# Performance work log

Measured on AMD Instinct MI355X. Metric: run time of the kernel, lower is better.

## Reference

```python
import jax, jax.numpy as jnp
import numpy as np

B, S, H, NH = 4, 1024, 2048, 16
D = H // NH  # head_dim = 128


def setup_inputs() -> dict:
    key = jax.random.key(0)
    ks = jax.random.split(key, 10)
    # RoPE tables: angle[t, j] = t * 10000^(-2j/D), cos/sin of the complex freqs_cis
    t = jnp.arange(S, dtype=jnp.float32)
    inv_freq = 1.0 / (10000.0 ** (jnp.arange(0, D, 2, dtype=jnp.float32) / D))
    ang = t[:, None] * inv_freq[None, :]  # [S, D//2]
    w = 0.02
    return {
        "hidden_states": jax.random.normal(ks[0], (B, S, H), jnp.float32),
        "freqs_cos": jnp.cos(ang),
        "freqs_sin": jnp.sin(ang),
        "attention_mask": jnp.ones((B, 1, 1, S), jnp.float32),
        "Wq": jax.random.normal(ks[1], (H, H), jnp.float32) * w,
        "bq": jnp.zeros((H,), jnp.float32),
        "Wk": jax.random.normal(ks[2], (H, H), jnp.float32) * w,
        "bk": jnp.zeros((H,), jnp.float32),
        "Wv": jax.random.normal(ks[3], (H, H), jnp.float32) * w,
        "bv": jnp.zeros((H,), jnp.float32),
        "Wo": jax.random.normal(ks[4], (H, H), jnp.float32) * w,
        "bo": jnp.zeros((H,), jnp.float32),
    }


def _rope(x, cos, sin):
    # x: [B, S, NH, D]; cos/sin: [S, D//2]. Complex multiply on (even, odd) pairs.
    x2 = x.reshape(x.shape[:-1] + (D // 2, 2))
    x0, x1 = x2[..., 0], x2[..., 1]
    c = cos[None, :, None, :]
    s = sin[None, :, None, :]
    o0 = x0 * c - x1 * s
    o1 = x0 * s + x1 * c
    return jnp.stack([o0, o1], axis=-1).reshape(x.shape)


def reference(hidden_states, freqs_cos, freqs_sin, attention_mask,
              Wq, bq, Wk, bk, Wv, bv, Wo, bo):
    b, s, _ = hidden_states.shape
    q = (hidden_states @ Wq.T + bq).reshape(b, s, NH, D)
    k = (hidden_states @ Wk.T + bk).reshape(b, s, NH, D)
    v = (hidden_states @ Wv.T + bv).reshape(b, s, NH, D)
    q = _rope(q, freqs_cos, freqs_sin)
    k = _rope(k, freqs_cos, freqs_sin)
    # scores: [b, h, q, k]; original scales by sqrt(embed_dim)=sqrt(hidden_size)
    scores = jnp.einsum('bqhd,bkhd->bhqk', q, k) / jnp.sqrt(jnp.float32(H))
    scores = jnp.where(attention_mask == 0, jnp.float32(-1e9), scores)
    probs = jax.nn.softmax(scores, axis=-1)  # dropout is identity in eval
    ctx = jnp.einsum('bhqk,bkhd->bqhd', probs, v).reshape(b, s, H)
    return ctx @ Wo.T + bo
```

## Files before the change

### kernel.cpp

```cpp
#include <hip/hip_runtime.h>
#include <stdint.h>

#define BATCH 4
#define SEQ   1024
#define NHEAD 16
#define DHEAD 128
#define HDIM  2048
#define GM    4096
#define GN    2048
#define GK    2048

typedef __attribute__((ext_vector_type(8)))  short    short8;
typedef __attribute__((ext_vector_type(4)))  float    f32x4;
typedef __attribute__((ext_vector_type(16))) float    f32x16;
typedef __attribute__((ext_vector_type(4)))  uint32_t u32x4;

__device__ __forceinline__ uint16_t f2bf(float f) {
  uint32_t u = __builtin_bit_cast(uint32_t, f);
  u += 0x7fffu + ((u >> 16) & 1u);
  return (uint16_t)(u >> 16);
}
__device__ __forceinline__ float bf2f(uint16_t h) {
  return __builtin_bit_cast(float, (uint32_t)h << 16);
}
__device__ __forceinline__ uint32_t cvtpk(float lo, float hi) {
  uint32_t r;
  asm("v_cvt_pk_bf16_f32 %0, %1, %2" : "=v"(r) : "v"(lo), "v"(hi));
  return r;
}

__device__ __forceinline__ uint32_t swz128(uint32_t a) { return a ^ (((a >> 7) & 7u) << 4); }
__device__ __forceinline__ uint32_t swz256(uint32_t a) { return a ^ (((a >> 8) & 7u) << 4); }

#define GAS __attribute__((address_space(1)))
#define LAS __attribute__((address_space(3)))
__device__ __forceinline__ void gload_lds16(const void* g, void* l) {
  __builtin_amdgcn_global_load_lds((GAS const void*)g, (LAS void*)l, 16, 0, 0);
}

__global__ void cvt_all_kernel(const float* __restrict__ hs,
                               const float* __restrict__ W0, const float* __restrict__ W1,
                               const float* __restrict__ W2, const float* __restrict__ W3,
                               uint16_t* __restrict__ Xbf, uint16_t* __restrict__ Wb) {
  const int bid = blockIdx.x;
  const float* src; uint16_t* dst;
  if (bid < 4096) {
    src = hs + (size_t)bid * 2048;
    dst = Xbf + (size_t)bid * 2048;
  } else {
    const int m = (bid - 4096) >> 11;
    const int blk = (bid - 4096) & 2047;
    const float* Ws = (m == 0) ? W0 : (m == 1) ? W1 : (m == 2) ? W2 : W3;
    src = Ws + (size_t)blk * 2048;
    dst = Wb + (size_t)m * HDIM * HDIM + (size_t)blk * 2048;
  }
  const float4* p = (const float4*)src + (size_t)threadIdx.x * 2;
  float4 a = p[0], b = p[1];
  uint32_t w0 = f2bf(a.x) | ((uint32_t)f2bf(a.y) << 16);
  uint32_t w1 = f2bf(a.z) | ((uint32_t)f2bf(a.w) << 16);
  uint32_t w2 = f2bf(b.x) | ((uint32_t)f2bf(b.y) << 16);
  uint32_t w3 = f2bf(b.z) | ((uint32_t)f2bf(b.w) << 16);
  int4 r; r.x = (int)w0; r.y = (int)w1; r.z = (int)w2; r.w = (int)w3;
  *(int4*)(dst + (size_t)threadIdx.x * 8) = r;
}

__global__ void rope_kernel(uint16_t* __restrict__ qb, uint16_t* __restrict__ kb,
                            const float* __restrict__ fcos, const float* __restrict__ fsin) {
  uint32_t i = blockIdx.x * 256 + threadIdx.x;
  uint16_t* p = (blockIdx.y == 0 ? qb : kb) + (size_t)i * 8;
  uint32_t e0 = i * 8;
  uint32_t row = e0 >> 11;
  uint32_t col = e0 & 2047;
  uint32_t s = row & (SEQ - 1);
  uint32_t pi = (col & (DHEAD - 1)) >> 1;
  float4 cv = *(const float4*)(fcos + (size_t)s * 64 + pi);
  float4 sv = *(const float4*)(fsin + (size_t)s * 64 + pi);
  int4 raw = *(const int4*)p;
  uint16_t u[8]; *(int4*)u = raw;
  float cc[4] = {cv.x, cv.y, cv.z, cv.w}, ss[4] = {sv.x, sv.y, sv.z, sv.w};
#pragma unroll
  for (int t = 0; t < 4; ++t) {
    float x0 = bf2f(u[2 * t]), x1 = bf2f(u[2 * t + 1]);
    float o0 = x0 * cc[t] - x1 * ss[t];
    float o1 = x0 * ss[t] + x1 * cc[t];
    u[2 * t] = f2bf(o0); u[2 * t + 1] = f2bf(o1);
  }
  *(int4*)p = *(int4*)u;
}

template <int MODE>
__device__ __forceinline__ void gemm_body(const uint16_t* __restrict__ A,
                                          const uint16_t* __restrict__ Bw,
                                          const float* __restrict__ bias,
                                          void* __restrict__ Cout) {
  __shared__ __align__(16) char smA[128 * 128];
  __shared__ __align__(16) char smB[128 * 128];
  const int tid = threadIdx.x, lane = tid & 63, wid = tid >> 6;
  const int c = lane & 15, g = lane >> 4;
  const int row0 = blockIdx.x * 128, col0 = blockIdx.y * 128;
  const int wr = wid >> 1, wc = wid & 1;
  f32x4 acc[4][4] = {};
  const uint32_t oBase = wid * 4096 + lane * 16;

  for (int kk = 0; kk < GK; kk += 64) {
#pragma unroll
    for (int q = 0; q < 4; ++q) {
      uint32_t o = oBase + q * 1024;
      uint32_t r = o >> 7;
      uint32_t cb = (o & 127) ^ ((r & 7u) << 4);
      gload_lds16((const char*)A + ((size_t)(row0 + r) * GK + kk) * 2 + cb,
                  smA + wid * 4096 + q * 1024);
      gload_lds16((const char*)Bw + ((size_t)(col0 + r) * GK + kk) * 2 + cb,
                  smB + wid * 4096 + q * 1024);
    }
    __syncthreads();
    short8 af[4][2], bf[4][2];
#pragma unroll
    for (int m = 0; m < 4; ++m) {
      const uint32_t row = (uint32_t)(wr * 64 + m * 16 + c);
#pragma unroll
      for (int ks = 0; ks < 2; ++ks)
        af[m][ks] = *(const short8*)(smA + row * 128 + (((uint32_t)(ks * 64 + g * 16)) ^ ((row & 7u) << 4)));
    }
#pragma unroll
    for (int n = 0; n < 4; ++n) {
      const uint32_t row = (uint32_t)(wc * 64 + n * 16 + c);
#pragma unroll
      for (int ks = 0; ks < 2; ++ks)
        bf[n][ks] = *(const short8*)(smB + row * 128 + (((uint32_t)(ks * 64 + g * 16)) ^ ((row & 7u) << 4)));
    }
#pragma unroll
    for (int m = 0; m < 4; ++m)
#pragma unroll
      for (int n = 0; n < 4; ++n)
#pragma unroll
        for (int ks = 0; ks < 2; ++ks)
          acc[m][n] = __builtin_amdgcn_mfma_f32_16x16x32_bf16(af[m][ks], bf[n][ks], acc[m][n], 0, 0, 0);
    __syncthreads();
  }

  float bn[4];
#pragma unroll
  for (int n = 0; n < 4; ++n) bn[n] = bias[col0 + wc * 64 + n * 16 + c];
#pragma unroll
  for (int m = 0; m < 4; ++m) {
    const int gr = row0 + wr * 64 + m * 16 + g * 4;
#pragma unroll
    for (int n = 0; n < 4; ++n) {
      const int gc = col0 + wc * 64 + n * 16 + c;
#pragma unroll
      for (int jj = 0; jj < 4; ++jj) {
        float v = acc[m][n][jj] + bn[n];
        if (MODE == 1) ((float*)Cout)[(size_t)(gr + jj) * GN + gc] = v;
        else           ((uint16_t*)Cout)[(size_t)(gr + jj) * GN + gc] = f2bf(v);
      }
    }
  }
}

__global__ __launch_bounds__(256, 2) void gemm_qkv_kernel(
    const uint16_t* __restrict__ X,
    const uint16_t* __restrict__ Wq, const uint16_t* __restrict__ Wk, const uint16_t* __restrict__ Wv,
    const float* __restrict__ bq, const float* __restrict__ bk, const float* __restrict__ bv,
    uint16_t* __restrict__ qo, uint16_t* __restrict__ ko, uint16_t* __restrict__ vo) {
  const uint16_t* W; const float* bias; uint16_t* out;
  if (blockIdx.z == 0)      { W = Wq; bias = bq; out = qo; }
  else if (blockIdx.z == 1) { W = Wk; bias = bk; out = ko; }
  else                      { W = Wv; bias = bv; out = vo; }
  gemm_body<0>(X, W, bias, out);
}

__global__ __launch_bounds__(256, 2) void gemm_out_kernel(
    const uint16_t* __restrict__ ctx, const uint16_t* __restrict__ Wo,
    const float* __restrict__ bo, float* __restrict__ out) {
  gemm_body<1>(ctx, Wo, bo, out);
}

__global__ __launch_bounds__(256, 2) void attn_kernel(
    const uint16_t* __restrict__ q, const uint16_t* __restrict__ k,
    const uint16_t* __restrict__ v, const float* __restrict__ mask,
    uint16_t* __restrict__ ctx) {
  __shared__ __align__(16) char pool[66048];
  float* smT = (float*)pool;

  const int tid = threadIdx.x, lane = tid & 63, wid = tid >> 6;
  const int c32 = lane & 31, hi = lane >> 5;
  const int lb = (blockIdx.x & 7) * 64 + (blockIdx.x >> 3);
  const int qt = lb & 7, bh = lb >> 3;
  const int h = bh & (NHEAD - 1), b = bh >> 4;
  const int q0 = qt * 128;
  const float scale = 0.022097086912079608f;

  short8 qreg[8];
  {
    const uint16_t* qrow = q + (size_t)(b * SEQ + q0 + wid * 32 + c32) * HDIM + h * DHEAD;
#pragma unroll
    for (int ks = 0; ks < 8; ++ks) qreg[ks] = *(const short8*)(qrow + ks * 16 + hi * 8);
  }

  const int kvg = tid >> 5;
  const int d0v = (tid & 31) * 4;

  auto issueK = [&](int s) {
    char* dK = pool + (s & 1) * 16384;
#pragma unroll
    for (int i = 0; i < 4; ++i) {
      uint32_t o_ = wid * 4096 + i * 1024 + lane * 16;
      uint32_t r = o_ >> 8;
      uint32_t cb = swz256(o_) & 255;
      gload_lds16((const char*)k + ((size_t)(b * SEQ + s * 64 + r) * HDIM + h * DHEAD) * 2 + cb,
                  dK + wid * 4096 + i * 1024);
    }
  };
  auto loadV = [&](int s, uint32_t vw[8][2]) {
    const uint16_t* vsrc = v + (size_t)(b * SEQ + s * 64 + kvg * 8) * HDIM + h * DHEAD + d0v;
#pragma unroll
    for (int e = 0; e < 8; ++e) {
      uint2 t2 = *(const uint2*)(vsrc + (size_t)e * HDIM);
      vw[e][0] = t2.x; vw[e][1] = t2.y;
    }
  };
  auto writeVT = [&](int s, uint32_t vw[8][2]) {
    char* dVT = pool + 32768 + (s & 1) * 16384;
#pragma unroll
    for (int j = 0; j < 4; ++j) {
      const int hw = j >> 1, sh = (j & 1) * 16;
      int4 pk;
      pk.x = (int)(((vw[0][hw] >> sh) & 0xffffu) | (((vw[1][hw] >> sh) & 0xffffu) << 16));
      pk.y = (int)(((vw[2][hw] >> sh) & 0xffffu) | (((vw[3][hw] >> sh) & 0xffffu) << 16));
      pk.z = (int)(((vw[4][hw] >> sh) & 0xffffu) | (((vw[5][hw] >> sh) & 0xffffu) << 16));
      pk.w = (int)(((vw[6][hw] >> sh) & 0xffffu) | (((vw[7][hw] >> sh) & 0xffffu) << 16));
      *(int4*)(dVT + swz128((uint32_t)((d0v + j) * 128 + kvg * 16))) = pk;
    }
  };

  float mreg = -1e30f, lreg = 0.f;
  f32x16 o[4] = {};

  {
    float mtmp = 0.f;
    if (tid < 64) mtmp = mask[b * SEQ + tid];
    uint32_t vw[8][2];
    loadV(0, vw);
    issueK(0);
    if (tid < 64) ((float*)(pool + 65536))[tid] = mtmp;
    writeVT(0, vw);
  }
  __syncthreads();

  for (int t = 0; t < 16; ++t) {
    const int cur = t & 1;
    const char* sK  = pool + cur * 16384;
    const char* sVT = pool + 32768 + cur * 16384;
    const float* smMaskF = (const float*)(pool + 65536 + cur * 256);

    float mtmp = 0.f;
    uint32_t vw[8][2];
    if (t < 15) {
      if (tid < 64) mtmp = mask[b * SEQ + (t + 1) * 64 + tid];
      loadV(t + 1, vw);
      issueK(t + 1);
    }

    f32x16 st[2] = {};
#pragma unroll
    for (int ks = 0; ks < 8; ++ks) {
#pragma unroll
      for (int mi = 0; mi < 2; ++mi) {
        const uint32_t row = (uint32_t)(mi * 32 + c32);
        short8 kf = *(const short8*)(sK + row * 256 +
                    (((uint32_t)(ks * 32 + hi * 16)) ^ ((row & 7u) << 4)));
        st[mi] = __builtin_amdgcn_mfma_f32_32x32x16_bf16(kf, qreg[ks], st[mi], 0, 0, 0);
      }
    }

    float p[32];
    float pmax = -1e30f;
#pragma unroll
    for (int mi = 0; mi < 2; ++mi) {
      const float* mb = smMaskF + mi * 32 + hi * 4;
      float4 m0 = *(const float4*)(mb);
      float4 m1 = *(const float4*)(mb + 8);
      float4 m2 = *(const float4*)(mb + 16);
      float4 m3 = *(const float4*)(mb + 24);
      float mm[16] = {m0.x, m0.y, m0.z, m0.w, m1.x, m1.y, m1.z, m1.w,
                      m2.x, m2.y, m2.z, m2.w, m3.x, m3.y, m3.z, m3.w};
#pragma unroll
      for (int r = 0; r < 16; ++r) {
        float s = st[mi][r] * scale;
        if (mm[r] == 0.f) s = -1e9f;
        p[mi * 16 + r] = s;
        pmax = fmaxf(pmax, s);
      }
    }
    pmax = fmaxf(pmax, __shfl_xor(pmax, 32, 64));

    if (!__all(pmax <= mreg + 8.f)) {
      float mnew = fmaxf(mreg, pmax);
      float fac = __expf(mreg - mnew);
      lreg *= fac;
#pragma unroll
      for (int dt = 0; dt < 4; ++dt)
#pragma unroll
        for (int e = 0; e < 16; ++e) o[dt][e] *= fac;
      mreg = mnew;
    }

    float rsum = 0.f;
    short8 pfrag[4];
#pragma unroll
    for (int mi = 0; mi < 2; ++mi) {
      float pe[16];
#pragma unroll
      for (int r = 0; r < 16; ++r) {
        pe[r] = __expf(p[mi * 16 + r] - mreg);
        rsum += pe[r];
      }
      uint32_t w[8], s[8];
#pragma unroll
      for (int j = 0; j < 8; ++j) w[j] = cvtpk(pe[2 * j], pe[2 * j + 1]);
#pragma unroll
      for (int j = 0; j < 8; ++j) s[j] = (uint32_t)__shfl_xor((int)w[j], 32, 64);
      u32x4 f0, f1;
      f0[0] = hi ? s[2] : w[0];  f0[1] = hi ? s[3] : w[1];
      f0[2] = hi ? w[2] : s[0];  f0[3] = hi ? w[3] : s[1];
      f1[0] = hi ? s[6] : w[4];  f1[1] = hi ? s[7] : w[5];
      f1[2] = hi ? w[6] : s[4];  f1[3] = hi ? w[7] : s[5];
      pfrag[mi * 2]     = __builtin_bit_cast(short8, f0);
      pfrag[mi * 2 + 1] = __builtin_bit_cast(short8, f1);
    }
    rsum += __shfl_xor(rsum, 32, 64);
    lreg += rsum;

    if (t < 15) {
      if (tid < 64) ((float*)(pool + 65536 + ((t + 1) & 1) * 256))[tid] = mtmp;
      writeVT(t + 1, vw);
    }

#pragma unroll
    for (int dt = 0; dt < 4; ++dt) {
      const uint32_t row = (uint32_t)(dt * 32 + c32);
#pragma unroll
      for (int e = 0; e < 4; ++e) {
        short8 vf = *(const short8*)(sVT + row * 128 +
                    (((uint32_t)(e * 32 + hi * 16)) ^ ((row & 7u) << 4)));
        o[dt] = __builtin_amdgcn_mfma_f32_32x32x16_bf16(vf, pfrag[e], o[dt], 0, 0, 0);
      }
    }

    __syncthreads();
  }

  const float linv = 1.f / lreg;
  float* myT = smT + wid * (32 * 36);
  const int qe = lane >> 1, de0 = (lane & 1) * 16;
#pragma unroll
  for (int dt = 0; dt < 4; ++dt) {
#pragma unroll
    for (int r = 0; r < 16; ++r) {
      const int drow = (r & 3) + 8 * (r >> 2) + 4 * hi;
      myT[c32 * 36 + drow] = o[dt][r] * linv;
    }
    float vv[16];
#pragma unroll
    for (int j = 0; j < 4; ++j) {
      float4 rd = *(const float4*)(myT + qe * 36 + de0 + j * 4);
      vv[j * 4 + 0] = rd.x; vv[j * 4 + 1] = rd.y; vv[j * 4 + 2] = rd.z; vv[j * 4 + 3] = rd.w;
    }
    uint32_t pw[8];
#pragma unroll
    for (int m = 0; m < 8; ++m)
      pw[m] = f2bf(vv[2 * m]) | ((uint32_t)f2bf(vv[2 * m + 1]) << 16);
    uint16_t* dst = ctx + (size_t)(b * SEQ + q0 + wid * 32 + qe) * HDIM + h * DHEAD + dt * 32 + de0;
    int4 s0; s0.x = (int)pw[0]; s0.y = (int)pw[1]; s0.z = (int)pw[2]; s0.w = (int)pw[3];
    int4 s1; s1.x = (int)pw[4]; s1.y = (int)pw[5]; s1.z = (int)pw[6]; s1.w = (int)pw[7];
    *(int4*)(dst) = s0;
    *(int4*)(dst + 8) = s1;
  }
}

extern "C" void kernel_launch(void* const* d_in, const int* in_sizes, int n_in,
                              void* d_out, int out_size, void* d_ws, size_t ws_size,
                              hipStream_t stream) {
  const float* hs   = (const float*)d_in[0];
  const float* fcos = (const float*)d_in[1];
  const float* fsin = (const float*)d_in[2];
  const float* mask = (const float*)d_in[3];
  const float* Wq = (const float*)d_in[4];  const float* bq = (const float*)d_in[5];
  const float* Wk = (const float*)d_in[6];  const float* bk = (const float*)d_in[7];
  const float* Wv = (const float*)d_in[8];  const float* bv = (const float*)d_in[9];
  const float* Wo = (const float*)d_in[10]; const float* bo = (const float*)d_in[11];
  float* out = (float*)d_out;

  char* ws = (char*)d_ws;
  const size_t XB = (size_t)GM * HDIM * 2;
  const size_t WB = (size_t)HDIM * HDIM * 2;
  uint16_t* Xbf = (uint16_t*)(ws);
  uint16_t* Wqb = (uint16_t*)(ws + XB);
  uint16_t* Wkb = (uint16_t*)(ws + XB + WB);
  uint16_t* Wvb = (uint16_t*)(ws + XB + 2 * WB);
  uint16_t* Wob = (uint16_t*)(ws + XB + 3 * WB);
  uint16_t* qb  = (uint16_t*)(ws + XB + 4 * WB);
  uint16_t* kb  = (uint16_t*)(ws + XB + 4 * WB + XB);
  uint16_t* vb  = (uint16_t*)(ws + XB + 4 * WB + 2 * XB);

  cvt_all_kernel<<<12288, 256, 0, stream>>>(hs, Wq, Wk, Wv, Wo, Xbf, Wqb);

  gemm_qkv_kernel<<<dim3(GM / 128, GN / 128, 3), 256, 0, stream>>>(
      Xbf, Wqb, Wkb, Wvb, bq, bk, bv, qb, kb, vb);

  rope_kernel<<<dim3((GM * HDIM) / 8 / 256, 2, 1), 256, 0, stream>>>(qb, kb, fcos, fsin);

  attn_kernel<<<512, 256, 0, stream>>>(qb, kb, vb, mask, Xbf);

  gemm_out_kernel<<<dim3(GM / 128, GN / 128, 1), 256, 0, stream>>>(Xbf, Wob, bo, out);
}
```

Measured before the change: 240.9 us.

## Process two 32-row query fragments per wave in attention kernel

Each attention block now handles 256 query rows instead of 128, with each wave keeping two Q fragments and two sets of softmax/output accumulators. Every K/V tile loaded into shared memory is reused across twice as many queries, halving K/V global traffic and LDS fill work per query. In exchange, register pressure doubles (launch bounds drop to one block per CU) and the grid shrinks to 256 blocks, which may underfill the 256 CUs and reduce latency hiding.

Result: slower. 252.1 us (+4.7%).

```diff
diff --git a/kernel.cpp b/kernel.cpp
--- a/kernel.cpp
+++ b/kernel.cpp
@@ -176,7 +176,7 @@
   gemm_body<1>(ctx, Wo, bo, out);
 }
 
-__global__ __launch_bounds__(256, 2) void attn_kernel(
+__global__ __launch_bounds__(256, 1) void attn_kernel(
     const uint16_t* __restrict__ q, const uint16_t* __restrict__ k,
     const uint16_t* __restrict__ v, const float* __restrict__ mask,
     uint16_t* __restrict__ ctx) {
@@ -185,17 +185,18 @@
 
   const int tid = threadIdx.x, lane = tid & 63, wid = tid >> 6;
   const int c32 = lane & 31, hi = lane >> 5;
-  const int lb = (blockIdx.x & 7) * 64 + (blockIdx.x >> 3);
-  const int qt = lb & 7, bh = lb >> 3;
+  const int lb = (blockIdx.x & 7) * 32 + (blockIdx.x >> 3);
+  const int qt = lb & 3, bh = lb >> 2;
   const int h = bh & (NHEAD - 1), b = bh >> 4;
-  const int q0 = qt * 128;
+  const int q0 = qt * 256;
   const float scale = 0.022097086912079608f;
 
-  short8 qreg[8];
-  {
-    const uint16_t* qrow = q + (size_t)(b * SEQ + q0 + wid * 32 + c32) * HDIM + h * DHEAD;
-#pragma unroll
-    for (int ks = 0; ks < 8; ++ks) qreg[ks] = *(const short8*)(qrow + ks * 16 + hi * 8);
+  short8 qreg[2][8];
+#pragma unroll
+  for (int f = 0; f < 2; ++f) {
+    const uint16_t* qrow = q + (size_t)(b * SEQ + q0 + wid * 64 + f * 32 + c32) * HDIM + h * DHEAD;
+#pragma unroll
+    for (int ks = 0; ks < 8; ++ks) qreg[f][ks] = *(const short8*)(qrow + ks * 16 + hi * 8);
   }
 
   const int kvg = tid >> 5;
@@ -234,8 +235,8 @@
     }
   };
 
-  float mreg = -1e30f, lreg = 0.f;
-  f32x16 o[4] = {};
+  float mreg[2] = {-1e30f, -1e30f}, lreg[2] = {0.f, 0.f};
+  f32x16 o[2][4] = {};
 
   {
     float mtmp = 0.f;
@@ -262,7 +263,7 @@
       issueK(t + 1);
     }
 
-    f32x16 st[2] = {};
+    f32x16 st[2][2] = {};
 #pragma unroll
     for (int ks = 0; ks < 8; ++ks) {
 #pragma unroll
@@ -270,12 +271,12 @@
         const uint32_t row = (uint32_t)(mi * 32 + c32);
         short8 kf = *(const short8*)(sK + row * 256 +
                     (((uint32_t)(ks * 32 + hi * 16)) ^ ((row & 7u) << 4)));
-        st[mi] = __builtin_amdgcn_mfma_f32_32x32x16_bf16(kf, qreg[ks], st[mi], 0, 0, 0);
-      }
-    }
-
-    float p[32];
-    float pmax = -1e30f;
+        st[0][mi] = __builtin_amdgcn_mfma_f32_32x32x16_bf16(kf, qreg[0][ks], st[0][mi], 0, 0, 0);
+        st[1][mi] = __builtin_amdgcn_mfma_f32_32x32x16_bf16(kf, qreg[1][ks], st[1][mi], 0, 0, 0);
+      }
+    }
+
+    float pmax[2] = {-1e30f, -1e30f};
 #pragma unroll
     for (int mi = 0; mi < 2; ++mi) {
       const float* mb = smMaskF + mi * 32 + hi * 4;
@@ -287,50 +288,60 @@
                       m2.x, m2.y, m2.z, m2.w, m3.x, m3.y, m3.z, m3.w};
 #pragma unroll
       for (int r = 0; r < 16; ++r) {
-        float s = st[mi][r] * scale;
-        if (mm[r] == 0.f) s = -1e9f;
-        p[mi * 16 + r] = s;
-        pmax = fmaxf(pmax, s);
-      }
-    }
-    pmax = fmaxf(pmax, __shfl_xor(pmax, 32, 64));
-
-    if (!__all(pmax <= mreg + 8.f)) {
-      float mnew = fmaxf(mreg, pmax);
-      float fac = __expf(mreg - mnew);
-      lreg *= fac;
-#pragma unroll
-      for (int dt = 0; dt < 4; ++dt)
-#pragma unroll
-        for (int e = 0; e < 16; ++e) o[dt][e] *= fac;
-      mreg = mnew;
-    }
-
-    float rsum = 0.f;
-    short8 pfrag[4];
-#pragma unroll
-    for (int mi = 0; mi < 2; ++mi) {
-      float pe[16];
-#pragma unroll
-      for (int r = 0; r < 16; ++r) {
-        pe[r] = __expf(p[mi * 16 + r] - mreg);
-        rsum += pe[r];
-      }
-      uint32_t w[8], s[8];
-#pragma unroll
-      for (int j = 0; j < 8; ++j) w[j] = cvtpk(pe[2 * j], pe[2 * j + 1]);
-#pragma unroll
-      for (int j = 0; j < 8; ++j) s[j] = (uint32_t)__shfl_xor((int)w[j], 32, 64);
-      u32x4 f0, f1;
-      f0[0] = hi ? s[2] : w[0];  f0[1] = hi ? s[3] : w[1];
-      f0[2] = hi ? w[2] : s[0];  f0[3] = hi ? w[3] : s[1];
-      f1[0] = hi ? s[6] : w[4];  f1[1] = hi ? s[7] : w[5];
-      f1[2] = hi ? w[6] : s[4];  f1[3] = hi ? w[7] : s[5];
-      pfrag[mi * 2]     = __builtin_bit_cast(short8, f0);
-      pfrag[mi * 2 + 1] = __builtin_bit_cast(short8, f1);
-    }
-    rsum += __shfl_xor(rsum, 32, 64);
-    lreg += rsum;
+#pragma unroll
+        for (int f = 0; f < 2; ++f) {
+          float s = st[f][mi][r] * scale;
+          if (mm[r] == 0.f) s = -1e9f;
+          st[f][mi][r] = s;
+          pmax[f] = fmaxf(pmax[f], s);
+        }
+      }
+    }
+    pmax[0] = fmaxf(pmax[0], __shfl_xor(pmax[0], 32, 64));
+    pmax[1] = fmaxf(pmax[1], __shfl_xor(pmax[1], 32, 64));
+
+    if (!__all((pmax[0] <= mreg[0] + 8.f) && (pmax[1] <= mreg[1] + 8.f))) {
+#pragma unroll
+      for (int f = 0; f < 2; ++f) {
+        float mnew = fmaxf(mreg[f], pmax[f]);
+        float fac = __expf(mreg[f] - mnew);
+        lreg[f] *= fac;
+#pragma unroll
+        for (int dt = 0; dt < 4; ++dt)
+#pragma unroll
+          for (int e = 0; e < 16; ++e) o[f][dt][e] *= fac;
+        mreg[f] = mnew;
+      }
+    }
+
+    short8 pfrag[2][4];
+#pragma unroll
+    for (int f = 0; f < 2; ++f) {
+      float rsum = 0.f;
+#pragma unroll
+      for (int mi = 0; mi < 2; ++mi) {
+        float pe[16];
+#pragma unroll
+        for (int r = 0; r < 16; ++r) {
+          pe[r] = __expf(st[f][mi][r] - mreg[f]);
+          rsum += pe[r];
+        }
+        uint32_t w[8], s[8];
+#pragma unroll
+        for (int j = 0; j < 8; ++j) w[j] = cvtpk(pe[2 * j], pe[2 * j + 1]);
+#pragma unroll
+        for (int j = 0; j < 8; ++j) s[j] = (uint32_t)__shfl_xor((int)w[j], 32, 64);
+        u32x4 f0, f1;
+        f0[0] = hi ? s[2] : w[0];  f0[1] = hi ? s[3] : w[1];
+        f0[2] = hi ? w[2] : s[0];  f0[3] = hi ? w[3] : s[1];
+        f1[0] = hi ? s[6] : w[4];  f1[1] = hi ? s[7] : w[5];
+        f1[2] = hi ? w[6] : s[4];  f1[3] = hi ? w[7] : s[5];
+        pfrag[f][mi * 2]     = __builtin_bit_cast(short8, f0);
+        pfrag[f][mi * 2 + 1] = __builtin_bit_cast(short8, f1);
+      }
+      rsum += __shfl_xor(rsum, 32, 64);
+      lreg[f] += rsum;
+    }
 
     if (t < 15) {
       if (tid < 64) ((float*)(pool + 65536 + ((t + 1) & 1) * 256))[tid] = mtmp;
@@ -344,38 +355,42 @@
       for (int e = 0; e < 4; ++e) {
         short8 vf = *(const short8*)(sVT + row * 128 +
                     (((uint32_t)(e * 32 + hi * 16)) ^ ((row & 7u) << 4)));
-        o[dt] = __builtin_amdgcn_mfma_f32_32x32x16_bf16(vf, pfrag[e], o[dt], 0, 0, 0);
+        o[0][dt] = __builtin_amdgcn_mfma_f32_32x32x16_bf16(vf, pfrag[0][e], o[0][dt], 0, 0, 0);
+        o[1][dt] = __builtin_amdgcn_mfma_f32_32x32x16_bf16(vf, pfrag[1][e], o[1][dt], 0, 0, 0);
       }
     }
 
     __syncthreads();
   }
 
-  const float linv = 1.f / lreg;
   float* myT = smT + wid * (32 * 36);
   const int qe = lane >> 1, de0 = (lane & 1) * 16;
 #pragma unroll
-  for (int dt = 0; dt < 4; ++dt) {
-#pragma unroll
-    for (int r = 0; r < 16; ++r) {
-      const int drow = (r & 3) + 8 * (r >> 2) + 4 * hi;
-      myT[c32 * 36 + drow] = o[dt][r] * linv;
-    }
-    float vv[16];
-#pragma unroll
-    for (int j = 0; j < 4; ++j) {
-      float4 rd = *(const float4*)(myT + qe * 36 + de0 + j * 4);
-      vv[j * 4 + 0] = rd.x; vv[j * 4 + 1] = rd.y; vv[j * 4 + 2] = rd.z; vv[j * 4 + 3] = rd.w;
-    }
-    uint32_t pw[8];
-#pragma unroll
-    for (int m = 0; m < 8; ++m)
-      pw[m] = f2bf(vv[2 * m]) | ((uint32_t)f2bf(vv[2 * m + 1]) << 16);
-    uint16_t* dst = ctx + (size_t)(b * SEQ + q0 + wid * 32 + qe) * HDIM + h * DHEAD + dt * 32 + de0;
-    int4 s0; s0.x = (int)pw[0]; s0.y = (int)pw[1]; s0.z = (int)pw[2]; s0.w = (int)pw[3];
-    int4 s1; s1.x = (int)pw[4]; s1.y = (int)pw[5]; s1.z = (int)pw[6]; s1.w = (int)pw[7];
-    *(int4*)(dst) = s0;
-    *(int4*)(dst + 8) = s1;
+  for (int f = 0; f < 2; ++f) {
+    const float linv = 1.f / lreg[f];
+#pragma unroll
+    for (int dt = 0; dt < 4; ++dt) {
+#pragma unroll
+      for (int r = 0; r < 16; ++r) {
+        const int drow = (r & 3) + 8 * (r >> 2) + 4 * hi;
+        myT[c32 * 36 + drow] = o[f][dt][r] * linv;
+      }
+      float vv[16];
+#pragma unroll
+      for (int j = 0; j < 4; ++j) {
+        float4 rd = *(const float4*)(myT + qe * 36 + de0 + j * 4);
+        vv[j * 4 + 0] = rd.x; vv[j * 4 + 1] = rd.y; vv[j * 4 + 2] = rd.z; vv[j * 4 + 3] = rd.w;
+      }
+      uint32_t pw[8];
+#pragma unroll
+      for (int m = 0; m < 8; ++m)
+        pw[m] = f2bf(vv[2 * m]) | ((uint32_t)f2bf(vv[2 * m + 1]) << 16);
+      uint16_t* dst = ctx + (size_t)(b * SEQ + q0 + wid * 64 + f * 32 + qe) * HDIM + h * DHEAD + dt * 32 + de0;
+      int4 s0; s0.x = (int)pw[0]; s0.y = (int)pw[1]; s0.z = (int)pw[2]; s0.w = (int)pw[3];
+      int4 s1; s1.x = (int)pw[4]; s1.y = (int)pw[5]; s1.z = (int)pw[6]; s1.w = (int)pw[7];
+      *(int4*)(dst) = s0;
+      *(int4*)(dst + 8) = s1;
+    }
   }
 }
 
@@ -411,7 +426,7 @@
 
   rope_kernel<<<dim3((GM * HDIM) / 8 / 256, 2, 1), 256, 0, stream>>>(qb, kb, fcos, fsin);
 
-  attn_kernel<<<512, 256, 0, stream>>>(qb, kb, vb, mask, Xbf);
+  attn_kernel<<<256, 256, 0, stream>>>(qb, kb, vb, mask, Xbf);
 
   gemm_out_kernel<<<dim3(GM / 128, GN / 128, 1), 256, 0, stream>>>(Xbf, Wob, bo, out);
 }
```
